# Kernel tuning notes

Hardware: AMD Instinct MI355X
Metric: run time of the kernel (lower is better)

## Reference

```python
import jax, jax.numpy as jnp
import numpy as np

B, S, DIN, DH = 8, 8192, 256, 256


def setup_inputs() -> dict:
    key = jax.random.key(0)
    k0, k1, k2, k3, k4 = jax.random.split(key, 5)
    stdv = 1.0 / np.sqrt(DIN)
    x = jax.random.normal(k0, (B, S, DIN), jnp.float32)
    W0 = jax.random.uniform(k1, (2 * DH, DIN), jnp.float32, -stdv, stdv)
    b0 = jax.random.uniform(k2, (2 * DH,), jnp.float32, -stdv, stdv)
    stdv2 = 1.0 / np.sqrt(DH)
    W1 = jax.random.uniform(k3, (2 * DH, DH), jnp.float32, -stdv2, stdv2)
    b1 = jax.random.uniform(k4, (2 * DH,), jnp.float32, -stdv2, stdv2)
    return {"x": x, "W0": W0, "b0": b0, "W1": W1, "b1": b1}


def _log_g(x):
    # log of g(x) = x + 0.5 for x >= 0 else sigmoid(x)
    return jnp.where(x >= 0, jnp.log(jax.nn.relu(x) + 0.5), -jax.nn.softplus(-x))


def _mingru_layer(x, W, b):
    # x: (B,S,Din); W: (2*DH, Din); b: (2*DH,)
    gh = jnp.einsum('bsd,ed->bse', x, W) + b          # (B,S,2*DH)
    gate, hidden = jnp.split(gh, 2, axis=-1)          # each (B,S,DH)
    log_coeffs = -jax.nn.softplus(gate)               # log(1 - z)
    log_vals = -jax.nn.softplus(-gate) + _log_g(hidden)  # log z + log h_tilde
    Bb, Ss, Dd = log_coeffs.shape
    # initial hidden h0 = g(0) = 0.5  ->  log(h0) = log(0.5)
    log_h0 = jnp.full((Bb, 1, Dd), jnp.log(0.5), log_coeffs.dtype)
    log_values = jnp.concatenate([log_h0, log_vals], axis=1)          # (B,S+1,DH)
    a_star = jnp.concatenate(
        [jnp.zeros((Bb, 1, Dd), log_coeffs.dtype), jnp.cumsum(log_coeffs, axis=1)],
        axis=1)                                                       # (B,S+1,DH)
    log_h = a_star + jax.lax.cumlogsumexp(log_values - a_star, axis=1)
    return jnp.exp(log_h)[:, 1:]                                      # (B,S,DH)


def reference(x, W0, b0, W1, b1):
    out0 = _mingru_layer(x, W0, b0)
    out1 = _mingru_layer(out0, W1, b1)
    h = jnp.stack([out0[:, -1:], out1[:, -1:]])  # (num_layers,B,1,DH)
    return out1, h
```

## Files before the change

### kernel.cpp

```cpp
#include <hip/hip_runtime.h>
#include <hip/hip_bf16.h>

#define Bb 8
#define Ss 8192
#define Dd 256
#define Mm (Bb * Ss)
#define Nn 512
#define NCHUNK 128
#define CLEN (Ss / NCHUNK)

typedef __hip_bfloat16 bf16;
typedef __attribute__((ext_vector_type(8))) short short8;
typedef __attribute__((ext_vector_type(4))) float f32x4;

__device__ __forceinline__ void load_lds16(const void* g, void* l) {
  __builtin_amdgcn_global_load_lds(
      (const __attribute__((address_space(1))) void*)g,
      (__attribute__((address_space(3))) void*)l, 16, 0, 0);
}

template <int N>
__device__ __forceinline__ void wait_vmcnt() {
  if constexpr (N == 0)
    asm volatile("s_waitcnt vmcnt(0)" ::: "memory");
  else if constexpr (N == 4)
    asm volatile("s_waitcnt vmcnt(4)" ::: "memory");
  else if constexpr (N == 6)
    asm volatile("s_waitcnt vmcnt(6)" ::: "memory");
  else
    static_assert(N == 0 || N == 4 || N == 6, "unsupported vmcnt");
}

__global__ __launch_bounds__(256) void cvt_f32_bf16(const float* __restrict__ in,
                                                    bf16* __restrict__ out,
                                                    long n4) {
  long i = (long)blockIdx.x * blockDim.x + threadIdx.x;
  if (i >= n4) return;
  const float4 v = ((const float4*)in)[i];
  union { ushort4 u; bf16 h[4]; } o;
  o.h[0] = __float2bfloat16(v.x);
  o.h[1] = __float2bfloat16(v.y);
  o.h[2] = __float2bfloat16(v.z);
  o.h[3] = __float2bfloat16(v.w);
  ((ushort4*)out)[i] = o.u;
}

__device__ __forceinline__ void av_from_gh(float gate, float hid, float& a,
                                           float& v) {
  gate = fminf(fmaxf(gate, -20.f), 20.f);
  float eg = __expf(gate);
  a = 1.f / (1.f + eg);
  float z = eg * a;
  float gfun;
  if (hid >= 0.f) {
    gfun = hid + 0.5f;
  } else {
    float eh = __expf(fmaxf(hid, -20.f));
    gfun = eh / (1.f + eh);
  }
  v = z * gfun;
}

__device__ __forceinline__ unsigned pack_av(float a, float v) {
  union { bf16 h[2]; unsigned u; } o;
  o.h[0] = __float2bfloat16(a);
  o.h[1] = __float2bfloat16(v);
  return o.u;
}

template <bool F32A>
__global__ __launch_bounds__(256) void gemm_av_fused(
    const void* __restrict__ Xv, const bf16* __restrict__ W,
    const float* __restrict__ bias, unsigned* __restrict__ AV,
    float* __restrict__ Asum, float* __restrict__ Vsum) {
  constexpr int ABY = F32A ? 16384 : 8192;
  constexpr int NLD = F32A ? 6 : 4;
  __shared__ __align__(16) char sm[2 * ABY + 16384];
  char* Abuf0 = sm;
  char* Abuf1 = sm + ABY;
  bf16* Bbuf0 = (bf16*)(sm + 2 * ABY);
  bf16* Bbuf1 = (bf16*)(sm + 2 * ABY + 8192);
  unsigned* Ts = (unsigned*)sm;

  const int tid = threadIdx.x;
  const int w = tid >> 6;
  const int l = tid & 63;
  const int fl = l & 15;
  const int q = l >> 4;

  const int id = blockIdx.x;
  const int lin = ((id & 7) << 8) | (id >> 3);
  const int cb = lin & 3;
  const int bt = lin >> 2;
  const long rowBase = (long)bt * 128;
  const int wrow = (w >> 1) * 64;
  const int wc = (w & 1) * 32;

  const float* Xf = (const float*)Xv;
  const bf16* Xb = (const bf16*)Xv;

  auto stageA = [&](char* dst, int k0) {
    if constexpr (F32A) {
#pragma unroll
      for (int c = 0; c < 4; c++) {
        const int L = c * 256 + tid;
        const int row = L >> 3;
        const int kc = (L & 7) ^ (row & 7);
        load_lds16(Xf + (rowBase + row) * 256 + k0 + kc * 4,
                   dst + (c * 256 + w * 64) * 16);
      }
    } else {
#pragma unroll
      for (int c = 0; c < 2; c++) {
        const int L = c * 256 + tid;
        const int row = L >> 2;
        const int kc = (L & 3) ^ ((row >> 1) & 3);
        load_lds16(Xb + (rowBase + row) * 256 + k0 + kc * 8,
                   dst + (c * 256 + w * 64) * 16);
      }
    }
  };
  auto stageB = [&](bf16* dst, int k0) {
#pragma unroll
    for (int c = 0; c < 2; c++) {
      const int L = c * 256 + tid;
      const int row = L >> 2;
      const int kc = (L & 3) ^ ((row >> 1) & 3);
      const int grow = (row < 64) ? (cb * 64 + row) : (192 + cb * 64 + row);
      load_lds16(W + (long)grow * 256 + k0 + kc * 8,
                 (char*)dst + (c * 256 + w * 64) * 16);
    }
  };

  auto fragA = [&](const char* buf, int mt) -> short8 {
    const int row = wrow + 16 * mt + fl;
    if constexpr (F32A) {
      const float* p = (const float*)buf + row * 32;
      const int k0c = (2 * q) ^ (row & 7);
      const int k1c = (2 * q + 1) ^ (row & 7);
      const float4 u0 = *(const float4*)(p + k0c * 4);
      const float4 u1 = *(const float4*)(p + k1c * 4);
      const float vals[8] = {u0.x, u0.y, u0.z, u0.w, u1.x, u1.y, u1.z, u1.w};
      short8 r;
#pragma unroll
      for (int i = 0; i < 8; i++) {
        union { bf16 h; short s; } t;
        t.h = __float2bfloat16(vals[i]);
        r[i] = t.s;
      }
      return r;
    } else {
      const int kc = q ^ ((row >> 1) & 3);
      return *(const short8*)((const bf16*)buf + row * 32 + kc * 8);
    }
  };
  auto fragB = [&](const bf16* buf, int nt) -> short8 {
    const int row =
        (nt < 2) ? (wc + 16 * nt + fl) : (64 + wc + 16 * (nt - 2) + fl);
    const int kc = q ^ ((row >> 1) & 3);
    return *(const short8*)(buf + row * 32 + kc * 8);
  };

  f32x4 acc[4][4];
#pragma unroll
  for (int i = 0; i < 4; i++)
#pragma unroll
    for (int j = 0; j < 4; j++) acc[i][j] = (f32x4)0.0f;

  stageA(Abuf0, 0);
  stageB(Bbuf0, 0);
  stageA(Abuf1, 32);
  stageB(Bbuf1, 32);
#pragma unroll
  for (int ks = 0; ks < 8; ks++) {
    char* Ac = (ks & 1) ? Abuf1 : Abuf0;
    bf16* Bc = (ks & 1) ? Bbuf1 : Bbuf0;
    if (ks < 7)
      wait_vmcnt<NLD>();
    else
      wait_vmcnt<0>();
    __builtin_amdgcn_s_barrier();
    __builtin_amdgcn_sched_barrier(0);
    short8 af[4], bf_[4];
#pragma unroll
    for (int mt = 0; mt < 4; mt++) af[mt] = fragA(Ac, mt);
#pragma unroll
    for (int nt = 0; nt < 4; nt++) bf_[nt] = fragB(Bc, nt);
#pragma unroll
    for (int mt = 0; mt < 4; mt++)
#pragma unroll
      for (int nt = 0; nt < 4; nt++)
        acc[mt][nt] = __builtin_amdgcn_mfma_f32_16x16x32_bf16(
            af[mt], bf_[nt], acc[mt][nt], 0, 0, 0);
    asm volatile("s_waitcnt lgkmcnt(0)" ::: "memory");
    __builtin_amdgcn_s_barrier();
    if (ks < 6) {
      stageA(Ac, (ks + 2) * 32);
      stageB(Bc, (ks + 2) * 32);
    }
  }

  float bg[2], bh[2];
#pragma unroll
  for (int p = 0; p < 2; p++) {
    const int d = cb * 64 + wc + 16 * p + fl;
    bg[p] = bias[d];
    bh[p] = bias[256 + d];
  }
  unsigned pk[4][2][4];
#pragma unroll
  for (int mt = 0; mt < 4; mt++) {
#pragma unroll
    for (int p = 0; p < 2; p++) {
      const int d = cb * 64 + wc + 16 * p + fl;
      const long r0 = rowBase + wrow + 16 * mt + q * 4;
#pragma unroll
      for (int r = 0; r < 4; r++) {
        float a, v;
        av_from_gh(acc[mt][p][r] + bg[p], acc[mt][p + 2][r] + bh[p], a, v);
        pk[mt][p][r] = pack_av(a, v);
        AV[(r0 + r) * 256 + d] = pk[mt][p][r];
      }
    }
  }

#pragma unroll
  for (int h = 0; h < 2; h++) {
    if ((w >> 1) == h) {
#pragma unroll
      for (int mt = 0; mt < 4; mt++)
#pragma unroll
        for (int p = 0; p < 2; p++)
#pragma unroll
          for (int r = 0; r < 4; r++)
            Ts[(16 * mt + 4 * q + r) * 65 + wc + 16 * p + fl] = pk[mt][p][r];
    }
    __syncthreads();
    if (tid < 64) {
      float A = 1.f, H = 0.f;
#pragma unroll 8
      for (int t = 0; t < 64; t++) {
        const unsigned p = Ts[t * 65 + tid];
        const float a = __uint_as_float((p & 0xffffu) << 16);
        const float v = __uint_as_float(p & 0xffff0000u);
        A *= a;
        H = a * H + v;
      }
      const long cg = (long)(bt >> 6) * NCHUNK + ((bt & 63) << 1) + h;
      Asum[cg * 256 + cb * 64 + tid] = A;
      Vsum[cg * 256 + cb * 64 + tid] = H;
    }
    __syncthreads();
  }
}

__global__ __launch_bounds__(256) void scan_combine(
    const float* __restrict__ Asum, const float* __restrict__ Vsum,
    float* __restrict__ Hin) {
  const int d = threadIdx.x;
  const int b = blockIdx.x;
  float h = 0.5f;
#pragma unroll 8
  for (int c = 0; c < NCHUNK; c++) {
    const long i = ((long)b * NCHUNK + c) * 256 + d;
    Hin[i] = h;
    h = Asum[i] * h + Vsum[i];
  }
}

template <bool WRITE_BF16>
__global__ __launch_bounds__(256) void scan_final(
    const unsigned* __restrict__ AV, const float* __restrict__ Hin,
    bf16* __restrict__ OutB, float* __restrict__ OutF,
    float* __restrict__ Hlast) {
  const int d = threadIdx.x;
  const int c = blockIdx.x % NCHUNK;
  const int b = blockIdx.x / NCHUNK;
  float h = Hin[(long)blockIdx.x * 256 + d];
  long base = ((long)b * Ss + (long)c * CLEN) * 256 + d;
#pragma unroll 8
  for (int t = 0; t < CLEN; t++) {
    const unsigned p = AV[base];
    const float a = __uint_as_float((p & 0xffffu) << 16);
    const float v = __uint_as_float(p & 0xffff0000u);
    h = a * h + v;
    if (WRITE_BF16)
      OutB[base] = __float2bfloat16(h);
    else
      OutF[base] = h;
    base += 256;
  }
  if (c == NCHUNK - 1) Hlast[b * 256 + d] = h;
}

extern "C" void kernel_launch(void* const* d_in, const int* in_sizes, int n_in,
                              void* d_out, int out_size, void* d_ws,
                              size_t ws_size, hipStream_t stream) {
  const float* x = (const float*)d_in[0];
  const float* W0f = (const float*)d_in[1];
  const float* b0 = (const float*)d_in[2];
  const float* W1f = (const float*)d_in[3];
  const float* b1 = (const float*)d_in[4];

  float* outF = (float*)d_out;
  float* hlast = outF + (long)Mm * 256;
  bf16* Xb = (bf16*)d_out;

  char* ws = (char*)d_ws;
  unsigned* AV = (unsigned*)ws;
  bf16* W0b = (bf16*)(ws + (long)Mm * 256 * 4);
  bf16* W1b = W0b + (long)Nn * Dd;
  float* Asum = (float*)(W1b + (long)Nn * Dd);
  float* Vsum = Asum + (long)Bb * NCHUNK * 256;
  float* Hin = Vsum + (long)Bb * NCHUNK * 256;

  const dim3 gemmGrid(2048);
  const dim3 blk(256);
  const dim3 scanGrid(Bb * NCHUNK);

  {
    const long n4w = (long)Nn * Dd / 4;
    cvt_f32_bf16<<<dim3((n4w + 255) / 256), blk, 0, stream>>>(W0f, W0b, n4w);
    cvt_f32_bf16<<<dim3((n4w + 255) / 256), blk, 0, stream>>>(W1f, W1b, n4w);
  }

  gemm_av_fused<true><<<gemmGrid, blk, 0, stream>>>(x, W0b, b0, AV, Asum,
                                                    Vsum);
  scan_combine<<<dim3(Bb), blk, 0, stream>>>(Asum, Vsum, Hin);
  scan_final<true><<<scanGrid, blk, 0, stream>>>(AV, Hin, Xb, nullptr, hlast);

  gemm_av_fused<false><<<gemmGrid, blk, 0, stream>>>(Xb, W1b, b1, AV, Asum,
                                                     Vsum);
  scan_combine<<<dim3(Bb), blk, 0, stream>>>(Asum, Vsum, Hin);
  scan_final<false><<<scanGrid, blk, 0, stream>>>(AV, Hin, nullptr, outF,
                                                  hlast + Bb * 256);
}
```

Baseline: 267.0 us.

## Pre-convert input to bf16, split chunk-carry scan into segments, tune GEMM occupancy

Layer 0's fp32 input now goes through a separate bf16 conversion pass, so a single bf16 GEMM kernel serves both layers. That GEMM precomputes its staging and fragment offsets and requests 5 blocks per CU. The serial 128-step carry combine becomes a two-level scheme: a parallel segment reduce, an 8-step scan, and a short per-chunk catch-up inside scan_final. Chunk summaries are packed as float2, and the activation branch is made branchless. The trade-off is an extra full pass over x, in exchange for shorter serial scan latency and a smaller LDS footprint in the GEMM.

```diff
diff --git a/kernel.cpp b/kernel.cpp
--- a/kernel.cpp
+++ b/kernel.cpp
@@ -8,6 +8,8 @@
 #define Nn 512
 #define NCHUNK 128
 #define CLEN (Ss / NCHUNK)
+#define NSEG 8
+#define SEGC (NCHUNK / NSEG)
 
 typedef __hip_bfloat16 bf16;
 typedef __attribute__((ext_vector_type(8))) short short8;
@@ -25,10 +27,8 @@
     asm volatile("s_waitcnt vmcnt(0)" ::: "memory");
   else if constexpr (N == 4)
     asm volatile("s_waitcnt vmcnt(4)" ::: "memory");
-  else if constexpr (N == 6)
-    asm volatile("s_waitcnt vmcnt(6)" ::: "memory");
   else
-    static_assert(N == 0 || N == 4 || N == 6, "unsupported vmcnt");
+    static_assert(N == 0 || N == 4, "unsupported vmcnt");
 }
 
 __global__ __launch_bounds__(256) void cvt_f32_bf16(const float* __restrict__ in,
@@ -51,13 +51,9 @@
   float eg = __expf(gate);
   a = 1.f / (1.f + eg);
   float z = eg * a;
-  float gfun;
-  if (hid >= 0.f) {
-    gfun = hid + 0.5f;
-  } else {
-    float eh = __expf(fmaxf(hid, -20.f));
-    gfun = eh / (1.f + eh);
-  }
+  float eh = __expf(fminf(fmaxf(hid, -20.f), 0.f));
+  float sig = eh / (1.f + eh);
+  float gfun = (hid >= 0.f) ? (hid + 0.5f) : sig;
   v = z * gfun;
 }
 
@@ -68,18 +64,13 @@
   return o.u;
 }
 
-template <bool F32A>
-__global__ __launch_bounds__(256) void gemm_av_fused(
-    const void* __restrict__ Xv, const bf16* __restrict__ W,
+__global__ __launch_bounds__(256, 5) void gemm_av_fused(
+    const bf16* __restrict__ X, const bf16* __restrict__ W,
     const float* __restrict__ bias, unsigned* __restrict__ AV,
-    float* __restrict__ Asum, float* __restrict__ Vsum) {
-  constexpr int ABY = F32A ? 16384 : 8192;
-  constexpr int NLD = F32A ? 6 : 4;
-  __shared__ __align__(16) char sm[2 * ABY + 16384];
-  char* Abuf0 = sm;
-  char* Abuf1 = sm + ABY;
-  bf16* Bbuf0 = (bf16*)(sm + 2 * ABY);
-  bf16* Bbuf1 = (bf16*)(sm + 2 * ABY + 8192);
+    float2* __restrict__ AVs) {
+  __shared__ __align__(16) char sm[32768];
+  bf16* Ab[2] = {(bf16*)sm, (bf16*)(sm + 8192)};
+  bf16* Bbf[2] = {(bf16*)(sm + 16384), (bf16*)(sm + 24576)};
   unsigned* Ts = (unsigned*)sm;
 
   const int tid = threadIdx.x;
@@ -96,70 +87,40 @@
   const int wrow = (w >> 1) * 64;
   const int wc = (w & 1) * 32;
 
-  const float* Xf = (const float*)Xv;
-  const bf16* Xb = (const bf16*)Xv;
-
-  auto stageA = [&](char* dst, int k0) {
-    if constexpr (F32A) {
-#pragma unroll
-      for (int c = 0; c < 4; c++) {
-        const int L = c * 256 + tid;
-        const int row = L >> 3;
-        const int kc = (L & 7) ^ (row & 7);
-        load_lds16(Xf + (rowBase + row) * 256 + k0 + kc * 4,
-                   dst + (c * 256 + w * 64) * 16);
-      }
-    } else {
-#pragma unroll
-      for (int c = 0; c < 2; c++) {
-        const int L = c * 256 + tid;
-        const int row = L >> 2;
-        const int kc = (L & 3) ^ ((row >> 1) & 3);
-        load_lds16(Xb + (rowBase + row) * 256 + k0 + kc * 8,
-                   dst + (c * 256 + w * 64) * 16);
-      }
-    }
+  const bf16* aSrc[2];
+  const bf16* bSrc[2];
+  int sDst[2];
+#pragma unroll
+  for (int c = 0; c < 2; c++) {
+    const int L = c * 256 + tid;
+    const int row = L >> 2;
+    const int kc = (L & 3) ^ ((row >> 1) & 3);
+    aSrc[c] = X + (rowBase + row) * 256 + kc * 8;
+    const int grow = (row < 64) ? (cb * 64 + row) : (192 + cb * 64 + row);
+    bSrc[c] = W + (long)grow * 256 + kc * 8;
+    sDst[c] = (c * 256 + w * 64) * 16;
+  }
+  auto stage = [&](int bi, int ks) {
+#pragma unroll
+    for (int c = 0; c < 2; c++)
+      load_lds16(aSrc[c] + ks * 32, (char*)Ab[bi] + sDst[c]);
+#pragma unroll
+    for (int c = 0; c < 2; c++)
+      load_lds16(bSrc[c] + ks * 32, (char*)Bbf[bi] + sDst[c]);
   };
-  auto stageB = [&](bf16* dst, int k0) {
-#pragma unroll
-    for (int c = 0; c < 2; c++) {
-      const int L = c * 256 + tid;
-      const int row = L >> 2;
-      const int kc = (L & 3) ^ ((row >> 1) & 3);
-      const int grow = (row < 64) ? (cb * 64 + row) : (192 + cb * 64 + row);
-      load_lds16(W + (long)grow * 256 + k0 + kc * 8,
-                 (char*)dst + (c * 256 + w * 64) * 16);
-    }
-  };
-
-  auto fragA = [&](const char* buf, int mt) -> short8 {
+
+  int aOff[4], bOff[4];
+#pragma unroll
+  for (int mt = 0; mt < 4; mt++) {
     const int row = wrow + 16 * mt + fl;
-    if constexpr (F32A) {
-      const float* p = (const float*)buf + row * 32;
-      const int k0c = (2 * q) ^ (row & 7);
-      const int k1c = (2 * q + 1) ^ (row & 7);
-      const float4 u0 = *(const float4*)(p + k0c * 4);
-      const float4 u1 = *(const float4*)(p + k1c * 4);
-      const float vals[8] = {u0.x, u0.y, u0.z, u0.w, u1.x, u1.y, u1.z, u1.w};
-      short8 r;
-#pragma unroll
-      for (int i = 0; i < 8; i++) {
-        union { bf16 h; short s; } t;
-        t.h = __float2bfloat16(vals[i]);
-        r[i] = t.s;
-      }
-      return r;
-    } else {
-      const int kc = q ^ ((row >> 1) & 3);
-      return *(const short8*)((const bf16*)buf + row * 32 + kc * 8);
-    }
-  };
-  auto fragB = [&](const bf16* buf, int nt) -> short8 {
+    aOff[mt] = row * 32 + (q ^ ((row >> 1) & 3)) * 8;
+  }
+#pragma unroll
+  for (int nt = 0; nt < 4; nt++) {
     const int row =
         (nt < 2) ? (wc + 16 * nt + fl) : (64 + wc + 16 * (nt - 2) + fl);
-    const int kc = q ^ ((row >> 1) & 3);
-    return *(const short8*)(buf + row * 32 + kc * 8);
-  };
+    bOff[nt] = row * 32 + (q ^ ((row >> 1) & 3)) * 8;
+  }
 
   f32x4 acc[4][4];
 #pragma unroll
@@ -167,25 +128,24 @@
 #pragma unroll
     for (int j = 0; j < 4; j++) acc[i][j] = (f32x4)0.0f;
 
-  stageA(Abuf0, 0);
-  stageB(Bbuf0, 0);
-  stageA(Abuf1, 32);
-  stageB(Bbuf1, 32);
+  stage(0, 0);
+  stage(1, 1);
 #pragma unroll
   for (int ks = 0; ks < 8; ks++) {
-    char* Ac = (ks & 1) ? Abuf1 : Abuf0;
-    bf16* Bc = (ks & 1) ? Bbuf1 : Bbuf0;
+    const int bi = ks & 1;
     if (ks < 7)
-      wait_vmcnt<NLD>();
+      wait_vmcnt<4>();
     else
       wait_vmcnt<0>();
     __builtin_amdgcn_s_barrier();
     __builtin_amdgcn_sched_barrier(0);
     short8 af[4], bf_[4];
 #pragma unroll
-    for (int mt = 0; mt < 4; mt++) af[mt] = fragA(Ac, mt);
-#pragma unroll
-    for (int nt = 0; nt < 4; nt++) bf_[nt] = fragB(Bc, nt);
+    for (int mt = 0; mt < 4; mt++)
+      af[mt] = *(const short8*)((const bf16*)Ab[bi] + aOff[mt]);
+#pragma unroll
+    for (int nt = 0; nt < 4; nt++)
+      bf_[nt] = *(const short8*)((const bf16*)Bbf[bi] + bOff[nt]);
 #pragma unroll
     for (int mt = 0; mt < 4; mt++)
 #pragma unroll
@@ -194,10 +154,8 @@
             af[mt], bf_[nt], acc[mt][nt], 0, 0, 0);
     asm volatile("s_waitcnt lgkmcnt(0)" ::: "memory");
     __builtin_amdgcn_s_barrier();
-    if (ks < 6) {
-      stageA(Ac, (ks + 2) * 32);
-      stageB(Bc, (ks + 2) * 32);
-    }
+    __builtin_amdgcn_sched_barrier(0);
+    if (ks < 6) stage(bi, ks + 2);
   }
 
   float bg[2], bh[2];
@@ -247,36 +205,54 @@
         H = a * H + v;
       }
       const long cg = (long)(bt >> 6) * NCHUNK + ((bt & 63) << 1) + h;
-      Asum[cg * 256 + cb * 64 + tid] = A;
-      Vsum[cg * 256 + cb * 64 + tid] = H;
+      AVs[cg * 256 + cb * 64 + tid] = make_float2(A, H);
     }
     __syncthreads();
   }
 }
 
-__global__ __launch_bounds__(256) void scan_combine(
-    const float* __restrict__ Asum, const float* __restrict__ Vsum,
-    float* __restrict__ Hin) {
+__global__ __launch_bounds__(256) void seg_reduce(
+    const float2* __restrict__ AVs, float2* __restrict__ Seg) {
+  const int d = threadIdx.x;
+  const int b = blockIdx.x >> 3;
+  const int s = blockIdx.x & 7;
+  float A = 1.f, H = 0.f;
+#pragma unroll
+  for (int j = 0; j < SEGC; j++) {
+    const float2 av = AVs[((long)b * NCHUNK + s * SEGC + j) * 256 + d];
+    H = av.x * H + av.y;
+    A *= av.x;
+  }
+  Seg[(b * NSEG + s) * 256 + d] = make_float2(A, H);
+}
+
+__global__ __launch_bounds__(256) void seg_scan(
+    const float2* __restrict__ Seg, float* __restrict__ Hseg) {
   const int d = threadIdx.x;
   const int b = blockIdx.x;
   float h = 0.5f;
-#pragma unroll 8
-  for (int c = 0; c < NCHUNK; c++) {
-    const long i = ((long)b * NCHUNK + c) * 256 + d;
-    Hin[i] = h;
-    h = Asum[i] * h + Vsum[i];
+#pragma unroll
+  for (int s = 0; s < NSEG; s++) {
+    Hseg[(b * NSEG + s) * 256 + d] = h;
+    const float2 sv = Seg[(b * NSEG + s) * 256 + d];
+    h = sv.x * h + sv.y;
   }
 }
 
 template <bool WRITE_BF16>
 __global__ __launch_bounds__(256) void scan_final(
-    const unsigned* __restrict__ AV, const float* __restrict__ Hin,
-    bf16* __restrict__ OutB, float* __restrict__ OutF,
-    float* __restrict__ Hlast) {
+    const unsigned* __restrict__ AV, const float2* __restrict__ AVs,
+    const float* __restrict__ Hseg, bf16* __restrict__ OutB,
+    float* __restrict__ OutF, float* __restrict__ Hlast) {
   const int d = threadIdx.x;
   const int c = blockIdx.x % NCHUNK;
   const int b = blockIdx.x / NCHUNK;
-  float h = Hin[(long)blockIdx.x * 256 + d];
+  const int s = c >> 4;
+  float h = Hseg[(b * NSEG + s) * 256 + d];
+  for (int j = s * SEGC; j < c; j++) {
+    const float2 av = AVs[((long)b * NCHUNK + j) * 256 + d];
+    h = av.x * h + av.y;
+  }
   long base = ((long)b * Ss + (long)c * CLEN) * 256 + d;
 #pragma unroll 8
   for (int t = 0; t < CLEN; t++) {
@@ -304,34 +280,37 @@
 
   float* outF = (float*)d_out;
   float* hlast = outF + (long)Mm * 256;
-  bf16* Xb = (bf16*)d_out;
+  bf16* X0b = (bf16*)d_out;
+  bf16* X1b = (bf16*)d_out + (long)Mm * 256;
 
   char* ws = (char*)d_ws;
   unsigned* AV = (unsigned*)ws;
   bf16* W0b = (bf16*)(ws + (long)Mm * 256 * 4);
   bf16* W1b = W0b + (long)Nn * Dd;
-  float* Asum = (float*)(W1b + (long)Nn * Dd);
-  float* Vsum = Asum + (long)Bb * NCHUNK * 256;
-  float* Hin = Vsum + (long)Bb * NCHUNK * 256;
+  float2* AVs = (float2*)(W1b + (long)Nn * Dd);
+  float2* Seg = AVs + (long)Bb * NCHUNK * 256;
+  float* Hseg = (float*)(Seg + (long)Bb * NSEG * 256);
 
   const dim3 gemmGrid(2048);
   const dim3 blk(256);
-  const dim3 scanGrid(Bb * NCHUNK);
 
   {
     const long n4w = (long)Nn * Dd / 4;
     cvt_f32_bf16<<<dim3((n4w + 255) / 256), blk, 0, stream>>>(W0f, W0b, n4w);
     cvt_f32_bf16<<<dim3((n4w + 255) / 256), blk, 0, stream>>>(W1f, W1b, n4w);
-  }
-
-  gemm_av_fused<true><<<gemmGrid, blk, 0, stream>>>(x, W0b, b0, AV, Asum,
-                                                    Vsum);
-  scan_combine<<<dim3(Bb), blk, 0, stream>>>(Asum, Vsum, Hin);
-  scan_final<true><<<scanGrid, blk, 0, stream>>>(AV, Hin, Xb, nullptr, hlast);
-
-  gemm_av_fused<false><<<gemmGrid, blk, 0, stream>>>(Xb, W1b, b1, AV, Asum,
-                                                     Vsum);
-  scan_combine<<<dim3(Bb), blk, 0, stream>>>(Asum, Vsum, Hin);
-  scan_final<false><<<scanGrid, blk, 0, stream>>>(AV, Hin, nullptr, outF,
-                                                  hlast + Bb * 256);
-}
+    const long n4x = (long)Mm * 256 / 4;
+    cvt_f32_bf16<<<dim3((n4x + 255) / 256), blk, 0, stream>>>(x, X0b, n4x);
+  }
+
+  gemm_av_fused<<<gemmGrid, blk, 0, stream>>>(X0b, W0b, b0, AV, AVs);
+  seg_reduce<<<dim3(Bb * NSEG), blk, 0, stream>>>(AVs, Seg);
+  seg_scan<<<dim3(Bb), blk, 0, stream>>>(Seg, Hseg);
+  scan_final<true><<<dim3(Bb * NCHUNK), blk, 0, stream>>>(AV, AVs, Hseg, X1b,
+                                                          nullptr, hlast);
+
+  gemm_av_fused<<<gemmGrid, blk, 0, stream>>>(X1b, W1b, b1, AV, AVs);
+  seg_reduce<<<dim3(Bb * NSEG), blk, 0, stream>>>(AVs, Seg);
+  seg_scan<<<dim3(Bb), blk, 0, stream>>>(Seg, Hseg);
+  scan_final<false><<<dim3(Bb * NCHUNK), blk, 0, stream>>>(
+      AV, AVs, Hseg, nullptr, outF, hlast + Bb * 256);
+}
```

After: 294.2 us. 1.1x slower.
